# Kernel optimization log

Measured on AMD Instinct MI355X. Metric: run time of the kernel, lower is better.

Reference implementation:

```python
import jax, jax.numpy as jnp
import numpy as np

NUM_HEADS = 12
HEAD_DIM = 64
HIDDEN = 768
QMAX = 127.0  # 8-bit symmetric
DOMAIN_MIN, DOMAIN_MAX = -10.0, 0.0
NUM_INTERVALS = 12


def _build_pla_coeffs():
    xs = np.linspace(DOMAIN_MIN, DOMAIN_MAX, 1001)
    ys = np.exp(xs)
    intervals = np.linspace(DOMAIN_MIN, DOMAIN_MAX, NUM_INTERVALS + 1)
    ms, cs = [], []
    for i in range(NUM_INTERVALS):
        a, b = intervals[i], intervals[i + 1]
        mask = (xs >= a) & (xs <= b)
        m, c = np.polyfit(xs[mask], ys[mask], 1)
        ms.append(m)
        cs.append(c)
    return (jnp.asarray(ms, jnp.float32), jnp.asarray(cs, jnp.float32),
            jnp.asarray(intervals, jnp.float32))

COEFFS_M, COEFFS_C, INTERVALS = _build_pla_coeffs()


def quantize(x):
    # per-row (last-dim) abs-max symmetric 8-bit fake quant
    max_val = jnp.max(jnp.abs(x), axis=-1, keepdims=True)
    scale = max_val / QMAX
    scale = jnp.where(scale == 0, 1.0, scale)
    return jnp.clip(jnp.round(x / scale), -QMAX, QMAX) * scale


def to_fixed_point(x, bits=32, frac_bits=26):
    scale = 2.0 ** frac_bits
    lo = -2.0 ** (bits - 1)
    hi = 2.0 ** (bits - 1) - 1
    return jnp.clip(jnp.round(x * scale), lo, hi) / scale


def pla_exp(x):
    xc = jnp.clip(x, DOMAIN_MIN, DOMAIN_MAX)
    # sum(x >= intervals) - 1 == searchsorted(intervals, x, 'right') - 1
    idx = jnp.clip(jnp.searchsorted(INTERVALS, xc, side='right') - 1, 0, NUM_INTERVALS - 1)
    return COEFFS_M[idx] * xc + COEFFS_C[idx]


def pla_softmax(scores):
    shifted = scores - jnp.max(scores, axis=-1, keepdims=True)
    shifted_fx = to_fixed_point(shifted, 32, 26)
    exps = pla_exp(shifted_fx)
    sm = exps / (jnp.sum(exps, axis=-1, keepdims=True) + 1e-9)
    return quantize(sm)


def q_linear(x, W, b):
    # QuantizedLinear: quantize input and weight (per-row), fp bias
    return quantize(x) @ quantize(W).T + b


def split_heads(x):
    B, S, _ = x.shape
    return x.reshape(B, S, NUM_HEADS, HEAD_DIM).transpose(0, 2, 1, 3)  # bhsd


def mhsa(hidden_states, Wq, bq, Wk, bk, Wv, bv, Wo, bo):
    B, S, H = hidden_states.shape
    scale = HEAD_DIM ** -0.5
    q = split_heads(q_linear(hidden_states, Wq, bq))
    k = split_heads(q_linear(hidden_states, Wk, bk))
    v = split_heads(q_linear(hidden_states, Wv, bv))
    # per-row quantization makes tile-wise quant identical to full quant
    scores = jnp.einsum('bhqd,bhkd->bhqk', quantize(q), quantize(k)) * scale
    probs = pla_softmax(scores)
    ctx = jnp.einsum('bhqk,bhkd->bhqd', probs, quantize(v))
    ctx = ctx.transpose(0, 2, 1, 3).reshape(B, S, H)
    return q_linear(ctx, Wo, bo)


def setup_inputs() -> dict:
    key = jax.random.key(0)
    ks = jax.random.split(key, 9)
    B, S = 8, 512
    hs = jax.random.normal(ks[0], (B, S, HIDDEN), dtype=jnp.float32)
    def w(k):
        return jax.random.normal(k, (HIDDEN, HIDDEN), dtype=jnp.float32) * 0.02
    def b(k):
        return jax.random.normal(k, (HIDDEN,), dtype=jnp.float32) * 0.02
    return {
        'hidden_states': hs,
        'Wq': w(ks[1]), 'bq': b(ks[2]),
        'Wk': w(ks[3]), 'bk': b(ks[4]),
        'Wv': w(ks[5]), 'bv': b(ks[6]),
        'Wo': w(ks[7]), 'bo': b(ks[8]),
    }


def reference(hidden_states, Wq, bq, Wk, bk, Wv, bv, Wo, bo):
    return mhsa(hidden_states, Wq, bq, Wk, bk, Wv, bv, Wo, bo)
```

## Files before the change

kernel.cpp:

```cpp
#include <hip/hip_runtime.h>
#include <cmath>

#define R_TOT 4096
#define HID   768
#define NHEAD 12
#define HDIM  64
#define SEQ   512
#define BATCH 8

typedef int   v4i  __attribute__((ext_vector_type(4)));
typedef float v4f  __attribute__((ext_vector_type(4)));
typedef _Float16 half8 __attribute__((ext_vector_type(8)));
typedef _Float16 half4v __attribute__((ext_vector_type(4)));

__device__ __forceinline__ void gl_lds16(const signed char* g, signed char* l) {
  __builtin_amdgcn_global_load_lds(
      (const __attribute__((address_space(1))) void*)g,
      (__attribute__((address_space(3))) void*)l, 16, 0, 0);
}

struct PlaConsts { float m[12]; float c[12]; float b[13]; };

static PlaConsts build_pla() {
  PlaConsts pc;
  const int NPTS = 1001;
  static double xs[NPTS], ys[NPTS];
  const double step = 10.0 / 1000.0;
  for (int j = 0; j < NPTS; ++j) xs[j] = (double)j * step + (-10.0);
  xs[NPTS - 1] = 0.0;
  for (int j = 0; j < NPTS; ++j) ys[j] = std::exp(xs[j]);
  double bnd[13];
  const double step2 = 10.0 / 12.0;
  for (int k = 0; k < 13; ++k) bnd[k] = (double)k * step2 + (-10.0);
  bnd[12] = 0.0;
  for (int i = 0; i < 12; ++i) {
    const double a = bnd[i], bb = bnd[i + 1];
    double sx = 0, sy = 0; int n = 0;
    for (int j = 0; j < NPTS; ++j)
      if (xs[j] >= a && xs[j] <= bb) { sx += xs[j]; sy += ys[j]; ++n; }
    const double xm = sx / n, ym = sy / n;
    double sxx = 0, sxy = 0;
    for (int j = 0; j < NPTS; ++j)
      if (xs[j] >= a && xs[j] <= bb) {
        const double dx = xs[j] - xm;
        sxx += dx * dx; sxy += dx * (ys[j] - ym);
      }
    const double m = sxy / sxx;
    pc.m[i] = (float)m;
    pc.c[i] = (float)(ym - m * xm);
  }
  for (int k = 0; k < 13; ++k) pc.b[k] = (float)bnd[k];
  return pc;
}
static const PlaConsts g_pla = build_pla();

__device__ __forceinline__ void quant_row_body(const float* __restrict__ x,
                                               signed char* __restrict__ qrow,
                                               float* __restrict__ srow) {
  const float v0 = x[threadIdx.x];
  const float v1 = x[threadIdx.x + 256];
  const float v2 = x[threadIdx.x + 512];
  float m = fmaxf(fmaxf(fabsf(v0), fabsf(v1)), fabsf(v2));
  #pragma unroll
  for (int off = 32; off; off >>= 1) m = fmaxf(m, __shfl_xor(m, off));
  __shared__ float red[4];
  const int lane = threadIdx.x & 63, wv = threadIdx.x >> 6;
  if (lane == 0) red[wv] = m;
  __syncthreads();
  if (threadIdx.x == 0) {
    float mm = fmaxf(fmaxf(red[0], red[1]), fmaxf(red[2], red[3]));
    float s = mm / 127.0f;
    if (s == 0.f) s = 1.f;
    red[0] = s;
    *srow = s;
  }
  __syncthreads();
  const float s = red[0];
  qrow[threadIdx.x] =
      (signed char)(int)fminf(fmaxf(rintf(v0 / s), -127.f), 127.f);
  qrow[threadIdx.x + 256] =
      (signed char)(int)fminf(fmaxf(rintf(v1 / s), -127.f), 127.f);
  qrow[threadIdx.x + 512] =
      (signed char)(int)fminf(fmaxf(rintf(v2 / s), -127.f), 127.f);
}

__global__ __launch_bounds__(256)
void quant_rows(const float* __restrict__ src,
                signed char* __restrict__ qout, float* __restrict__ sout) {
  const int row = blockIdx.x;
  quant_row_body(src + (size_t)row * HID, qout + (size_t)row * HID, sout + row);
}

__global__ __launch_bounds__(256)
void quant_all(const float* hs, const float* w0, const float* w1,
               const float* w2, const float* w3,
               signed char* qx, float* sx,
               signed char* q0, signed char* q1, signed char* q2, signed char* q3,
               float* s0, float* s1, float* s2, float* s3) {
  const int bid = blockIdx.x;
  const float* src; signed char* qo; float* so; int row;
  if (bid < R_TOT)            { src = hs; qo = qx; so = sx; row = bid; }
  else if (bid < R_TOT + 768) { src = w0; qo = q0; so = s0; row = bid - R_TOT; }
  else if (bid < R_TOT + 1536){ src = w1; qo = q1; so = s1; row = bid - R_TOT - 768; }
  else if (bid < R_TOT + 2304){ src = w2; qo = q2; so = s2; row = bid - R_TOT - 1536; }
  else                        { src = w3; qo = q3; so = s3; row = bid - R_TOT - 2304; }
  quant_row_body(src + (size_t)row * HID, qo + (size_t)row * HID, so + row);
}

__device__ __forceinline__
void proj_body(int mode,
               const signed char* __restrict__ qx, const float* __restrict__ sx,
               const signed char* __restrict__ qw, const float* __restrict__ sw,
               const float* __restrict__ bias,
               signed char* __restrict__ qo, float* __restrict__ so,
               _Float16* __restrict__ vt, float* __restrict__ fo,
               signed char* Al, signed char* Bl) {
  const int tid = threadIdx.x;
  const int w = tid >> 6, lane = tid & 63;
  const int n = lane & 15, quad = lane >> 4;
  const int row0 = blockIdx.x * 128, col0 = blockIdx.y * 64;
  const int lr = lane >> 3;
  const int lc = lane & 7;
  const int cg = lc ^ lr;
  v4i acc[2][4];
  #pragma unroll
  for (int s = 0; s < 2; ++s)
    #pragma unroll
    for (int j = 0; j < 4; ++j) acc[s][j] = (v4i){0, 0, 0, 0};
  for (int k0 = 0; k0 < HID; k0 += 128) {
    if (k0) __syncthreads();
    #pragma unroll
    for (int m = 0; m < 4; ++m) {
      const int ci = w * 4 + m;
      gl_lds16(qx + (size_t)(row0 + ci * 8 + lr) * HID + k0 + cg * 16,
               Al + ci * 1024);
    }
    #pragma unroll
    for (int m = 0; m < 2; ++m) {
      const int ci = w * 2 + m;
      gl_lds16(qw + (size_t)(col0 + ci * 8 + lr) * HID + k0 + cg * 16,
               Bl + ci * 1024);
    }
    __syncthreads();
    #pragma unroll
    for (int ks4 = 0; ks4 < 8; ks4 += 4) {
      const int sw16 = ((quad + ks4) ^ (n & 7)) * 16;
      const v4i af0 = *(const v4i*)&Al[(w * 16 + n) * 128 + sw16];
      const v4i af1 = *(const v4i*)&Al[(64 + w * 16 + n) * 128 + sw16];
      #pragma unroll
      for (int j = 0; j < 4; ++j) {
        const v4i bf = *(const v4i*)&Bl[(j * 16 + n) * 128 + sw16];
        acc[0][j] = __builtin_amdgcn_mfma_i32_16x16x64_i8(af0, bf, acc[0][j], 0, 0, 0);
        acc[1][j] = __builtin_amdgcn_mfma_i32_16x16x64_i8(af1, bf, acc[1][j], 0, 0, 0);
      }
    }
  }
  float swc4[4], bc4[4];
  #pragma unroll
  for (int j = 0; j < 4; ++j) {
    swc4[j] = sw[col0 + j * 16 + n];
    bc4[j] = bias[col0 + j * 16 + n];
  }
  #pragma unroll
  for (int s = 0; s < 2; ++s) {
    const int mrow = s * 64 + w * 16 + quad * 4;
    float sxr[4];
    #pragma unroll
    for (int r = 0; r < 4; ++r) sxr[r] = sx[row0 + mrow + r];
    float vals[4][4];
    #pragma unroll
    for (int j = 0; j < 4; ++j)
      #pragma unroll
      for (int r = 0; r < 4; ++r)
        vals[j][r] = (float)acc[s][j][r] * (sxr[r] * swc4[j]) + bc4[j];
    if (mode == 1) {
      const int h = blockIdx.y;
      #pragma unroll
      for (int r = 0; r < 4; ++r) {
        float m = 0.f;
        #pragma unroll
        for (int j = 0; j < 4; ++j) m = fmaxf(m, fabsf(vals[j][r]));
        #pragma unroll
        for (int off = 1; off < 16; off <<= 1) m = fmaxf(m, __shfl_xor(m, off));
        float sq = m / 127.0f;
        if (sq == 0.f) sq = 1.f;
        const int grow = row0 + mrow + r;
        const int bidx = grow >> 9, sidx = grow & 511;
        const size_t rowidx = ((size_t)bidx * NHEAD + h) * SEQ + sidx;
        #pragma unroll
        for (int j = 0; j < 4; ++j) {
          float q = fminf(fmaxf(rintf(vals[j][r] / sq), -127.f), 127.f);
          qo[rowidx * HDIM + j * 16 + n] = (signed char)(int)q;
        }
        if (n == 0) so[rowidx] = sq;
      }
    } else if (mode == 2) {
      const int h = blockIdx.y;
      float srow[4];
      #pragma unroll
      for (int r = 0; r < 4; ++r) {
        float m = 0.f;
        #pragma unroll
        for (int j = 0; j < 4; ++j) m = fmaxf(m, fabsf(vals[j][r]));
        #pragma unroll
        for (int off = 1; off < 16; off <<= 1) m = fmaxf(m, __shfl_xor(m, off));
        float sq = m / 127.0f;
        if (sq == 0.f) sq = 1.f;
        srow[r] = sq;
      }
      const int grow0 = row0 + mrow;
      const int bidx = grow0 >> 9, sidx = grow0 & 511;
      const int kb = sidx >> 5, ko = sidx & 31;
      const size_t hbv = (size_t)bidx * NHEAD + h;
      #pragma unroll
      for (int j = 0; j < 4; ++j) {
        half4v hv;
        #pragma unroll
        for (int r = 0; r < 4; ++r) {
          float q = fminf(fmaxf(rintf(vals[j][r] / srow[r]), -127.f), 127.f);
          hv[r] = (_Float16)(q * srow[r]);
        }
        *(half4v*)(vt + ((hbv * 16 + kb) * 64 + j * 16 + n) * 32 + ko) = hv;
      }
    } else {
      #pragma unroll
      for (int r = 0; r < 4; ++r) {
        const size_t base = (size_t)(row0 + mrow + r) * HID + col0;
        #pragma unroll
        for (int j = 0; j < 4; ++j)
          fo[base + j * 16 + n] = vals[j][r];
      }
    }
  }
}

__global__ __launch_bounds__(256)
void proj_qkv(const signed char* __restrict__ qx, const float* __restrict__ sx,
              const signed char* qwq, const float* swq, const float* bq,
              signed char* qqd, float* qqs,
              const signed char* qwk, const float* swk, const float* bk,
              signed char* qkd, float* qks,
              const signed char* qwv, const float* swv, const float* bv,
              _Float16* vt2) {
  __shared__ __align__(16) signed char Al[128 * 128];
  __shared__ __align__(16) signed char Bl[64 * 128];
  if (blockIdx.z == 0)
    proj_body(1, qx, sx, qwq, swq, bq, qqd, qqs, nullptr, nullptr, Al, Bl);
  else if (blockIdx.z == 1)
    proj_body(1, qx, sx, qwk, swk, bk, qkd, qks, nullptr, nullptr, Al, Bl);
  else
    proj_body(2, qx, sx, qwv, swv, bv, nullptr, nullptr, vt2, nullptr, Al, Bl);
}

__global__ __launch_bounds__(256)
void proj_out(const signed char* __restrict__ qx, const float* __restrict__ sx,
              const signed char* qw, const float* sw, const float* bias,
              float* fo) {
  __shared__ __align__(16) signed char Al[128 * 128];
  __shared__ __align__(16) signed char Bl[64 * 128];
  proj_body(0, qx, sx, qw, sw, bias, nullptr, nullptr, nullptr, fo, Al, Bl);
}

__device__ __forceinline__
void softmax_exp_tile(float (&s)[8][4], float mx26, const float4* __restrict__ pt4,
                      float& sum_out, float& amax_out) {
  float sum = 0.f, amax = 0.f;
  #pragma unroll
  for (int t = 0; t < 8; ++t) {
    #pragma unroll
    for (int r = 0; r < 4; ++r) {
      float sh = s[t][r] - mx26;
      sh = fmaxf(sh, -671088640.0f);
      const float tq = rintf(sh);
      const float xc = tq * 1.4901161193847656e-08f;
      int g = (int)((xc + 10.0f) * 1.2f);
      g = g > 11 ? 11 : g;
      float4 E = pt4[g];
      int gn = g + ((xc >= E.y) ? 1 : 0) - ((xc < E.x) ? 1 : 0);
      gn = gn < 0 ? 0 : (gn > 11 ? 11 : gn);
      if (gn != g) E = pt4[gn];
      const float e = __fadd_rn(__fmul_rn(E.z, xc), E.w);
      s[t][r] = e;
      sum += e;
      amax = fmaxf(amax, fabsf(e));
    }
  }
  sum += __shfl_xor(sum, 16);
  sum += __shfl_xor(sum, 32);
  amax = fmaxf(amax, __shfl_xor(amax, 16));
  amax = fmaxf(amax, __shfl_xor(amax, 32));
  sum_out = sum; amax_out = amax;
}

__device__ __forceinline__
void quant_pack_tile(const float (&s)[8][4], float t127,
                     _Float16* __restrict__ phtrow, int w, int quad) {
  #pragma unroll
  for (int t = 0; t < 8; ++t) {
    half4v hq;
    #pragma unroll
    for (int r = 0; r < 4; ++r) {
      const float qf = fminf(fmaxf(rintf(s[t][r] * t127), -127.f), 127.f);
      hq[r] = (_Float16)qf;
    }
    *(half4v*)&phtrow[(t * 4 + w) * 16 + quad * 4] = hq;
  }
}

__device__ __forceinline__
v4f pv_tile(const _Float16* __restrict__ vbase, const _Float16* __restrict__ prow) {
  v4f acc = {0.f, 0.f, 0.f, 0.f};
  #pragma unroll
  for (int kt = 0; kt < 16; ++kt) {
    const half8 bf = *(const half8*)(vbase + kt * 2048);
    acc = __builtin_amdgcn_mfma_f32_16x16x32_f16(*(const half8*)(prow + kt * 32), bf, acc, 0, 0, 0);
  }
  return acc;
}

#define PSTR 520
__global__ __launch_bounds__(256)
void attn_kernel(const signed char* __restrict__ qq, const float* __restrict__ qss,
                 const signed char* __restrict__ qk, const float* __restrict__ kss,
                 const _Float16* __restrict__ vt2,
                 float* __restrict__ ctx, const PlaConsts pc) {
  __shared__ __align__(16) _Float16 PhT[2][16 * PSTR];
  __shared__ __align__(16) float red_max[2][16][4];
  __shared__ __align__(16) float red_sum[2][16][4];
  __shared__ __align__(16) float red_amax[2][16][4];
  __shared__ float psa[2][16];
  __shared__ __align__(16) float4 pt4[12];

  const int tid = threadIdx.x;
  const int q0 = blockIdx.x * 32;
  const int hh = blockIdx.y, bz = blockIdx.z;
  const size_t hb = (size_t)bz * NHEAD + hh;
  const signed char* qqh = qq + (hb * SEQ + q0) * HDIM;
  const signed char* qkh = qk + hb * SEQ * HDIM;
  const float* ksp = kss + hb * SEQ;

  if (tid < 12)
    pt4[tid] = make_float4(pc.b[tid], pc.b[tid + 1], pc.m[tid], pc.c[tid]);

  const int w = tid >> 6, lane = tid & 63;
  const int n = lane & 15, quad = lane >> 4;

  float s26[2][8][4];
  {
    const v4i qf0 = *(const v4i*)(qqh + (size_t)n * HDIM + quad * 16);
    const v4i qf1 = *(const v4i*)(qqh + (size_t)(16 + n) * HDIM + quad * 16);
    const float qs0 = (qss[hb * SEQ + q0 + n] * 0.125f) * 67108864.0f;
    const float qs1 = (qss[hb * SEQ + q0 + 16 + n] * 0.125f) * 67108864.0f;
    float vmax0 = -3.0e38f, vmax1 = -3.0e38f;
    #pragma unroll
    for (int t = 0; t < 8; ++t) {
      const int kc0 = (t * 4 + w) * 16;
      const v4i kfrag = *(const v4i*)(qkh + (size_t)(kc0 + n) * HDIM + quad * 16);
      const float4 ks4 = *(const float4*)(ksp + kc0 + quad * 4);
      v4i zero = {};
      const v4i a0 = __builtin_amdgcn_mfma_i32_16x16x64_i8(kfrag, qf0, zero, 0, 0, 0);
      const v4i a1 = __builtin_amdgcn_mfma_i32_16x16x64_i8(kfrag, qf1, zero, 0, 0, 0);
      const float ks[4] = {ks4.x, ks4.y, ks4.z, ks4.w};
      #pragma unroll
      for (int r = 0; r < 4; ++r) {
        const float v0 = (float)a0[r] * (qs0 * ks[r]);
        const float v1 = (float)a1[r] * (qs1 * ks[r]);
        s26[0][t][r] = v0; vmax0 = fmaxf(vmax0, v0);
        s26[1][t][r] = v1; vmax1 = fmaxf(vmax1, v1);
      }
    }
    vmax0 = fmaxf(vmax0, __shfl_xor(vmax0, 16));
    vmax0 = fmaxf(vmax0, __shfl_xor(vmax0, 32));
    vmax1 = fmaxf(vmax1, __shfl_xor(vmax1, 16));
    vmax1 = fmaxf(vmax1, __shfl_xor(vmax1, 32));
    if (quad == 0) { red_max[0][n][w] = vmax0; red_max[1][n][w] = vmax1; }
  }
  __syncthreads();

  {
    const float4 rm = *(const float4*)&red_max[0][n][0];
    const float mx26 = fmaxf(fmaxf(rm.x, rm.y), fmaxf(rm.z, rm.w));
    float sum, amax;
    softmax_exp_tile(s26[0], mx26, pt4, sum, amax);
    if (quad == 0) { red_sum[0][n][w] = sum; red_amax[0][n][w] = amax; }
  }
  __syncthreads();

  {
    const float4 rs = *(const float4*)&red_sum[0][n][0];
    const float4 ra = *(const float4*)&red_amax[0][n][0];
    float denom = (rs.x + rs.y) + (rs.z + rs.w);
    denom = __fadd_rn(denom, 1e-9f);
    const float rden = 1.0f / denom;
    const float am = fmaxf(fmaxf(ra.x, ra.y), fmaxf(ra.z, ra.w));
    float ps = (am * rden) / 127.0f;
    if (ps == 0.f) ps = 1.f;
    if (w == 0 && quad == 0) psa[0][n] = ps;
    const float t127 = 127.0f / am;
    quant_pack_tile(s26[0], t127, &PhT[0][n * PSTR], w, quad);

    const float4 rm = *(const float4*)&red_max[1][n][0];
    const float mx26 = fmaxf(fmaxf(rm.x, rm.y), fmaxf(rm.z, rm.w));
    float sum, amax;
    softmax_exp_tile(s26[1], mx26, pt4, sum, amax);
    if (quad == 0) { red_sum[1][n][w] = sum; red_amax[1][n][w] = amax; }
  }
  __syncthreads();

  const _Float16* vbase = vt2 + ((size_t)hb * 16 * 64 + (w * 16 + n)) * 32 + quad * 8;

  {
    const v4f acc0 = pv_tile(vbase, &PhT[0][n * PSTR + quad * 8]);

    const float4 rs = *(const float4*)&red_sum[1][n][0];
    const float4 ra = *(const float4*)&red_amax[1][n][0];
    float denom = (rs.x + rs.y) + (rs.z + rs.w);
    denom = __fadd_rn(denom, 1e-9f);
    const float rden = 1.0f / denom;
    const float am = fmaxf(fmaxf(ra.x, ra.y), fmaxf(ra.z, ra.w));
    float ps = (am * rden) / 127.0f;
    if (ps == 0.f) ps = 1.f;
    if (w == 0 && quad == 0) psa[1][n] = ps;
    const float t127 = 127.0f / am;
    quant_pack_tile(s26[1], t127, &PhT[1][n * PSTR], w, quad);

    #pragma unroll
    for (int r = 0; r < 4; ++r) {
      const int row = quad * 4 + r;
      ctx[((size_t)bz * SEQ + q0 + row) * HID + (size_t)hh * HDIM + w * 16 + n] =
          acc0[r] * psa[0][row];
    }
  }
  __syncthreads();

  {
    const v4f acc1 = pv_tile(vbase, &PhT[1][n * PSTR + quad * 8]);
    #pragma unroll
    for (int r = 0; r < 4; ++r) {
      const int row = quad * 4 + r;
      ctx[((size_t)bz * SEQ + q0 + 16 + row) * HID + (size_t)hh * HDIM + w * 16 + n] =
          acc1[r] * psa[1][row];
    }
  }
}

extern "C" void kernel_launch(void* const* d_in, const int* in_sizes, int n_in,
                              void* d_out, int out_size, void* d_ws, size_t ws_size,
                              hipStream_t stream) {
  (void)in_sizes; (void)n_in; (void)out_size; (void)ws_size;
  const float* hs = (const float*)d_in[0];
  const float* Wq = (const float*)d_in[1];
  const float* bq = (const float*)d_in[2];
  const float* Wk = (const float*)d_in[3];
  const float* bk = (const float*)d_in[4];
  const float* Wv = (const float*)d_in[5];
  const float* bv = (const float*)d_in[6];
  const float* Wo = (const float*)d_in[7];
  const float* bo = (const float*)d_in[8];
  float* out = (float*)d_out;

  char* ws = (char*)d_ws;
  size_t off = 0;
  auto alloc = [&](size_t bytes) -> char* {
    char* p = ws + off;
    off += (bytes + 255) & ~(size_t)255;
    return p;
  };
  signed char* qx  = (signed char*)alloc((size_t)R_TOT * HID);
  float*       sx  = (float*)alloc((size_t)R_TOT * 4);
  signed char* qwq = (signed char*)alloc((size_t)HID * HID);
  signed char* qwk = (signed char*)alloc((size_t)HID * HID);
  signed char* qwv = (signed char*)alloc((size_t)HID * HID);
  signed char* qwo = (signed char*)alloc((size_t)HID * HID);
  float*       swq = (float*)alloc((size_t)HID * 4);
  float*       swk = (float*)alloc((size_t)HID * 4);
  float*       swv = (float*)alloc((size_t)HID * 4);
  float*       swo = (float*)alloc((size_t)HID * 4);
  signed char* qqd = (signed char*)alloc((size_t)R_TOT * HID);
  float*       qqs = (float*)alloc((size_t)BATCH * NHEAD * SEQ * 4);
  signed char* qkd = (signed char*)alloc((size_t)R_TOT * HID);
  float*       qks = (float*)alloc((size_t)BATCH * NHEAD * SEQ * 4);
  float*       ctx = (float*)alloc((size_t)R_TOT * HID * 4);
  _Float16*    vt2 = (_Float16*)alloc((size_t)BATCH * NHEAD * HDIM * SEQ * 2);
  signed char* qc  = qx;
  float*       scs = sx;

  quant_all<<<R_TOT + 4 * HID, 256, 0, stream>>>(
      hs, Wq, Wk, Wv, Wo, qx, sx,
      qwq, qwk, qwv, qwo, swq, swk, swv, swo);

  proj_qkv<<<dim3(R_TOT / 128, HID / 64, 3), 256, 0, stream>>>(
      qx, sx, qwq, swq, bq, qqd, qqs,
      qwk, swk, bk, qkd, qks,
      qwv, swv, bv, vt2);

  attn_kernel<<<dim3(SEQ / 32, NHEAD, BATCH), 256, 0, stream>>>(
      qqd, qqs, qkd, qks, vt2, ctx, g_pla);

  quant_rows<<<R_TOT, 256, 0, stream>>>(ctx, qc, scs);
  proj_out<<<dim3(R_TOT / 128, HID / 64), 256, 0, stream>>>(
      qc, scs, qwo, swo, bo, out);
}
```

Measured before the change: 150.9 us.

## Quantize one row per wave and widen QKV projection tiles to two heads

Row quantization now runs one row per wavefront, using float4 loads and packed int8 stores. This removes the LDS reduction and both block barriers, and packs four rows into each block. The QKV projection is templated on the N-tile width and uses 128 columns (two heads) per block, which halves redundant A-tile loads and doubles MFMA work per A fragment. In exchange it doubles B-tile LDS to 32 KB total and raises accumulator register use, which may cut occupancy, and it halves the projection grid size.

```diff
diff --git a/kernel.cpp b/kernel.cpp
--- a/kernel.cpp
+++ b/kernel.cpp
@@ -54,41 +54,39 @@
 }
 static const PlaConsts g_pla = build_pla();
 
-__device__ __forceinline__ void quant_row_body(const float* __restrict__ x,
+__device__ __forceinline__ void quant_row_wave(const float* __restrict__ x,
                                                signed char* __restrict__ qrow,
                                                float* __restrict__ srow) {
-  const float v0 = x[threadIdx.x];
-  const float v1 = x[threadIdx.x + 256];
-  const float v2 = x[threadIdx.x + 512];
-  float m = fmaxf(fmaxf(fabsf(v0), fabsf(v1)), fabsf(v2));
+  const int lane = threadIdx.x & 63;
+  const float4* x4 = (const float4*)x;
+  const float4 a = x4[lane];
+  const float4 b = x4[lane + 64];
+  const float4 c = x4[lane + 128];
+  float m = fmaxf(fmaxf(fabsf(a.x), fabsf(a.y)), fmaxf(fabsf(a.z), fabsf(a.w)));
+  m = fmaxf(m, fmaxf(fmaxf(fabsf(b.x), fabsf(b.y)), fmaxf(fabsf(b.z), fabsf(b.w))));
+  m = fmaxf(m, fmaxf(fmaxf(fabsf(c.x), fabsf(c.y)), fmaxf(fabsf(c.z), fabsf(c.w))));
   #pragma unroll
   for (int off = 32; off; off >>= 1) m = fmaxf(m, __shfl_xor(m, off));
-  __shared__ float red[4];
-  const int lane = threadIdx.x & 63, wv = threadIdx.x >> 6;
-  if (lane == 0) red[wv] = m;
-  __syncthreads();
-  if (threadIdx.x == 0) {
-    float mm = fmaxf(fmaxf(red[0], red[1]), fmaxf(red[2], red[3]));
-    float s = mm / 127.0f;
-    if (s == 0.f) s = 1.f;
-    red[0] = s;
-    *srow = s;
-  }
-  __syncthreads();
-  const float s = red[0];
-  qrow[threadIdx.x] =
-      (signed char)(int)fminf(fmaxf(rintf(v0 / s), -127.f), 127.f);
-  qrow[threadIdx.x + 256] =
-      (signed char)(int)fminf(fmaxf(rintf(v1 / s), -127.f), 127.f);
-  qrow[threadIdx.x + 512] =
-      (signed char)(int)fminf(fmaxf(rintf(v2 / s), -127.f), 127.f);
+  float s = m / 127.0f;
+  if (s == 0.f) s = 1.f;
+  auto qb = [&](float v) -> int {
+    return ((int)fminf(fmaxf(rintf(v / s), -127.f), 127.f)) & 255;
+  };
+  const int p0 = qb(a.x) | (qb(a.y) << 8) | (qb(a.z) << 16) | (qb(a.w) << 24);
+  const int p1 = qb(b.x) | (qb(b.y) << 8) | (qb(b.z) << 16) | (qb(b.w) << 24);
+  const int p2 = qb(c.x) | (qb(c.y) << 8) | (qb(c.z) << 16) | (qb(c.w) << 24);
+  int* q4 = (int*)qrow;
+  q4[lane] = p0;
+  q4[lane + 64] = p1;
+  q4[lane + 128] = p2;
+  if (lane == 0) *srow = s;
 }
 
 __global__ __launch_bounds__(256)
 void quant_rows(const float* __restrict__ src,
                 signed char* __restrict__ qout, float* __restrict__ sout) {
-  const int row = blockIdx.x;
-  quant_row_body(src + (size_t)row * HID, qout + (size_t)row * HID, sout + row);
+  const int row = blockIdx.x * 4 + (threadIdx.x >> 6);
+  quant_row_wave(src + (size_t)row * HID, qout + (size_t)row * HID, sout + row);
 }
 
 __global__ __launch_bounds__(256)
@@ -97,16 +95,17 @@
                signed char* qx, float* sx,
                signed char* q0, signed char* q1, signed char* q2, signed char* q3,
                float* s0, float* s1, float* s2, float* s3) {
-  const int bid = blockIdx.x;
-  const float* src; signed char* qo; float* so; int row;
-  if (bid < R_TOT)            { src = hs; qo = qx; so = sx; row = bid; }
-  else if (bid < R_TOT + 768) { src = w0; qo = q0; so = s0; row = bid - R_TOT; }
-  else if (bid < R_TOT + 1536){ src = w1; qo = q1; so = s1; row = bid - R_TOT - 768; }
-  else if (bid < R_TOT + 2304){ src = w2; qo = q2; so = s2; row = bid - R_TOT - 1536; }
-  else                        { src = w3; qo = q3; so = s3; row = bid - R_TOT - 2304; }
-  quant_row_body(src + (size_t)row * HID, qo + (size_t)row * HID, so + row);
-}
-
+  const int row = blockIdx.x * 4 + (threadIdx.x >> 6);
+  const float* src; signed char* qo; float* so; int r;
+  if (row < R_TOT)             { src = hs; qo = qx; so = sx; r = row; }
+  else if (row < R_TOT + 768)  { src = w0; qo = q0; so = s0; r = row - R_TOT; }
+  else if (row < R_TOT + 1536) { src = w1; qo = q1; so = s1; r = row - R_TOT - 768; }
+  else if (row < R_TOT + 2304) { src = w2; qo = q2; so = s2; r = row - R_TOT - 1536; }
+  else                         { src = w3; qo = q3; so = s3; r = row - R_TOT - 2304; }
+  quant_row_wave(src + (size_t)r * HID, qo + (size_t)r * HID, so + r);
+}
+
+template <int NT>
 __device__ __forceinline__
 void proj_body(int mode,
                const signed char* __restrict__ qx, const float* __restrict__ sx,
@@ -118,15 +117,15 @@
   const int tid = threadIdx.x;
   const int w = tid >> 6, lane = tid & 63;
   const int n = lane & 15, quad = lane >> 4;
-  const int row0 = blockIdx.x * 128, col0 = blockIdx.y * 64;
+  const int row0 = blockIdx.x * 128, col0 = blockIdx.y * (NT * 16);
   const int lr = lane >> 3;
   const int lc = lane & 7;
   const int cg = lc ^ lr;
-  v4i acc[2][4];
+  v4i acc[2][NT];
   #pragma unroll
   for (int s = 0; s < 2; ++s)
     #pragma unroll
-    for (int j = 0; j < 4; ++j) acc[s][j] = (v4i){0, 0, 0, 0};
+    for (int j = 0; j < NT; ++j) acc[s][j] = (v4i){0, 0, 0, 0};
   for (int k0 = 0; k0 < HID; k0 += 128) {
     if (k0) __syncthreads();
     #pragma unroll
@@ -136,8 +135,8 @@
                Al + ci * 1024);
     }
     #pragma unroll
-    for (int m = 0; m < 2; ++m) {
-      const int ci = w * 2 + m;
+    for (int m = 0; m < NT / 2; ++m) {
+      const int ci = w * (NT / 2) + m;
       gl_lds16(qw + (size_t)(col0 + ci * 8 + lr) * HID + k0 + cg * 16,
                Bl + ci * 1024);
     }
@@ -148,18 +147,18 @@
       const v4i af0 = *(const v4i*)&Al[(w * 16 + n) * 128 + sw16];
       const v4i af1 = *(const v4i*)&Al[(64 + w * 16 + n) * 128 + sw16];
       #pragma unroll
-      for (int j = 0; j < 4; ++j) {
+      for (int j = 0; j < NT; ++j) {
         const v4i bf = *(const v4i*)&Bl[(j * 16 + n) * 128 + sw16];
         acc[0][j] = __builtin_amdgcn_mfma_i32_16x16x64_i8(af0, bf, acc[0][j], 0, 0, 0);
         acc[1][j] = __builtin_amdgcn_mfma_i32_16x16x64_i8(af1, bf, acc[1][j], 0, 0, 0);
       }
     }
   }
-  float swc4[4], bc4[4];
-  #pragma unroll
-  for (int j = 0; j < 4; ++j) {
-    swc4[j] = sw[col0 + j * 16 + n];
-    bc4[j] = bias[col0 + j * 16 + n];
+  float swcv[NT], bcv[NT];
+  #pragma unroll
+  for (int j = 0; j < NT; ++j) {
+    swcv[j] = sw[col0 + j * 16 + n];
+    bcv[j] = bias[col0 + j * 16 + n];
   }
   #pragma unroll
   for (int s = 0; s < 2; ++s) {
@@ -167,67 +166,73 @@
     float sxr[4];
     #pragma unroll
     for (int r = 0; r < 4; ++r) sxr[r] = sx[row0 + mrow + r];
-    float vals[4][4];
-    #pragma unroll
-    for (int j = 0; j < 4; ++j)
+    float vals[NT][4];
+    #pragma unroll
+    for (int j = 0; j < NT; ++j)
       #pragma unroll
       for (int r = 0; r < 4; ++r)
-        vals[j][r] = (float)acc[s][j][r] * (sxr[r] * swc4[j]) + bc4[j];
+        vals[j][r] = (float)acc[s][j][r] * (sxr[r] * swcv[j]) + bcv[j];
     if (mode == 1) {
-      const int h = blockIdx.y;
       #pragma unroll
-      for (int r = 0; r < 4; ++r) {
-        float m = 0.f;
+      for (int g = 0; g < NT / 4; ++g) {
+        const int h = col0 / HDIM + g;
         #pragma unroll
-        for (int j = 0; j < 4; ++j) m = fmaxf(m, fabsf(vals[j][r]));
+        for (int r = 0; r < 4; ++r) {
+          float m = 0.f;
+          #pragma unroll
+          for (int j = 0; j < 4; ++j) m = fmaxf(m, fabsf(vals[g * 4 + j][r]));
+          #pragma unroll
+          for (int off = 1; off < 16; off <<= 1) m = fmaxf(m, __shfl_xor(m, off));
+          float sq = m / 127.0f;
+          if (sq == 0.f) sq = 1.f;
+          const int grow = row0 + mrow + r;
+          const int bidx = grow >> 9, sidx = grow & 511;
+          const size_t rowidx = ((size_t)bidx * NHEAD + h) * SEQ + sidx;
+          #pragma unroll
+          for (int j = 0; j < 4; ++j) {
+            float q = fminf(fmaxf(rintf(vals[g * 4 + j][r] / sq), -127.f), 127.f);
+            qo[rowidx * HDIM + j * 16 + n] = (signed char)(int)q;
+          }
+          if (n == 0) so[rowidx] = sq;
+        }
+      }
+    } else if (mode == 2) {
+      #pragma unroll
+      for (int g = 0; g < NT / 4; ++g) {
+        const int h = col0 / HDIM + g;
+        float srow[4];
         #pragma unroll
-        for (int off = 1; off < 16; off <<= 1) m = fmaxf(m, __shfl_xor(m, off));
-        float sq = m / 127.0f;
-        if (sq == 0.f) sq = 1.f;
-        const int grow = row0 + mrow + r;
-        const int bidx = grow >> 9, sidx = grow & 511;
-        const size_t rowidx = ((size_t)bidx * NHEAD + h) * SEQ + sidx;
+        for (int r = 0; r < 4; ++r) {
+          float m = 0.f;
+          #pragma unroll
+          for (int j = 0; j < 4; ++j) m = fmaxf(m, fabsf(vals[g * 4 + j][r]));
+          #pragma unroll
+          for (int off = 1; off < 16; off <<= 1) m = fmaxf(m, __shfl_xor(m, off));
+          float sq = m / 127.0f;
+          if (sq == 0.f) sq = 1.f;
+          srow[r] = sq;
+        }
+        const int grow0 = row0 + mrow;
+        const int bidx = grow0 >> 9, sidx = grow0 & 511;
+        const int kb = sidx >> 5, ko = sidx & 31;
+        const size_t hbv = (size_t)bidx * NHEAD + h;
         #pragma unroll
         for (int j = 0; j < 4; ++j) {
-          float q = fminf(fmaxf(rintf(vals[j][r] / sq), -127.f), 127.f);
-          qo[rowidx * HDIM + j * 16 + n] = (signed char)(int)q;
+          half4v hv;
+          #pragma unroll
+          for (int r = 0; r < 4; ++r) {
+            float q = fminf(fmaxf(rintf(vals[g * 4 + j][r] / srow[r]), -127.f), 127.f);
+            hv[r] = (_Float16)(q * srow[r]);
+          }
+          *(half4v*)(vt + ((hbv * 16 + kb) * 64 + j * 16 + n) * 32 + ko) = hv;
         }
-        if (n == 0) so[rowidx] = sq;
-      }
-    } else if (mode == 2) {
-      const int h = blockIdx.y;
-      float srow[4];
-      #pragma unroll
-      for (int r = 0; r < 4; ++r) {
-        float m = 0.f;
-        #pragma unroll
-        for (int j = 0; j < 4; ++j) m = fmaxf(m, fabsf(vals[j][r]));
-        #pragma unroll
-        for (int off = 1; off < 16; off <<= 1) m = fmaxf(m, __shfl_xor(m, off));
-        float sq = m / 127.0f;
-        if (sq == 0.f) sq = 1.f;
-        srow[r] = sq;
-      }
-      const int grow0 = row0 + mrow;
-      const int bidx = grow0 >> 9, sidx = grow0 & 511;
-      const int kb = sidx >> 5, ko = sidx & 31;
-      const size_t hbv = (size_t)bidx * NHEAD + h;
-      #pragma unroll
-      for (int j = 0; j < 4; ++j) {
-        half4v hv;
-        #pragma unroll
-        for (int r = 0; r < 4; ++r) {
-          float q = fminf(fmaxf(rintf(vals[j][r] / srow[r]), -127.f), 127.f);
-          hv[r] = (_Float16)(q * srow[r]);
-        }
-        *(half4v*)(vt + ((hbv * 16 + kb) * 64 + j * 16 + n) * 32 + ko) = hv;
       }
     } else {
       #pragma unroll
       for (int r = 0; r < 4; ++r) {
         const size_t base = (size_t)(row0 + mrow + r) * HID + col0;
         #pragma unroll
-        for (int j = 0; j < 4; ++j)
+        for (int j = 0; j < NT; ++j)
           fo[base + j * 16 + n] = vals[j][r];
       }
     }
@@ -243,13 +248,13 @@
               const signed char* qwv, const float* swv, const float* bv,
               _Float16* vt2) {
   __shared__ __align__(16) signed char Al[128 * 128];
-  __shared__ __align__(16) signed char Bl[64 * 128];
+  __shared__ __align__(16) signed char Bl[128 * 128];
   if (blockIdx.z == 0)
-    proj_body(1, qx, sx, qwq, swq, bq, qqd, qqs, nullptr, nullptr, Al, Bl);
+    proj_body<8>(1, qx, sx, qwq, swq, bq, qqd, qqs, nullptr, nullptr, Al, Bl);
   else if (blockIdx.z == 1)
-    proj_body(1, qx, sx, qwk, swk, bk, qkd, qks, nullptr, nullptr, Al, Bl);
+    proj_body<8>(1, qx, sx, qwk, swk, bk, qkd, qks, nullptr, nullptr, Al, Bl);
   else
-    proj_body(2, qx, sx, qwv, swv, bv, nullptr, nullptr, vt2, nullptr, Al, Bl);
+    proj_body<8>(2, qx, sx, qwv, swv, bv, nullptr, nullptr, vt2, nullptr, Al, Bl);
 }
 
 __global__ __launch_bounds__(256)
@@ -258,7 +263,7 @@
               float* fo) {
   __shared__ __align__(16) signed char Al[128 * 128];
   __shared__ __align__(16) signed char Bl[64 * 128];
-  proj_body(0, qx, sx, qw, sw, bias, nullptr, nullptr, nullptr, fo, Al, Bl);
+  proj_body<4>(0, qx, sx, qw, sw, bias, nullptr, nullptr, nullptr, fo, Al, Bl);
 }
 
 __device__ __forceinline__
@@ -485,11 +490,11 @@
   signed char* qc  = qx;
   float*       scs = sx;
 
-  quant_all<<<R_TOT + 4 * HID, 256, 0, stream>>>(
+  quant_all<<<(R_TOT + 4 * HID) / 4, 256, 0, stream>>>(
       hs, Wq, Wk, Wv, Wo, qx, sx,
       qwq, qwk, qwv, qwo, swq, swk, swv, swo);
 
-  proj_qkv<<<dim3(R_TOT / 128, HID / 64, 3), 256, 0, stream>>>(
+  proj_qkv<<<dim3(R_TOT / 128, HID / 128, 3), 256, 0, stream>>>(
       qx, sx, qwq, swq, bq, qqd, qqs,
       qwk, swk, bk, qkd, qks,
       qwv, swv, bv, vt2);
@@ -497,7 +502,7 @@
   attn_kernel<<<dim3(SEQ / 32, NHEAD, BATCH), 256, 0, stream>>>(
       qqd, qqs, qkd, qks, vt2, ctx, g_pla);
 
-  quant_rows<<<R_TOT, 256, 0, stream>>>(ctx, qc, scs);
+  quant_rows<<<R_TOT / 4, 256, 0, stream>>>(ctx, qc, scs);
   proj_out<<<dim3(R_TOT / 128, HID / 64), 256, 0, stream>>>(
       qc, scs, qwo, swo, bo, out);
 }
```

New measurement: 156.0 us. 1.03x slower.
